# Performance work log

Measured on AMD Instinct MI355X. Metric: run time of the kernel, lower is better.

Reference implementation:

```python
import jax, jax.numpy as jnp
import numpy as np

N = 50000      # nodes
D = 64         # hidden
EMB = 16       # emb_dims
E = 800000     # edges = N * knn(16)
R2 = 0.3 ** 2  # r^2 at epoch 0
GW = 1.0       # grav_weight at epoch 0
EPS = 1e-5


def _lin_params(k, fi, fo):
    kw, kb = jax.random.split(k)
    W = jax.random.normal(kw, (fi, fo), jnp.float32) / np.sqrt(fi).astype(np.float32)
    b = jax.random.normal(kb, (fo,), jnp.float32) * 0.01
    return W, b


def setup_inputs() -> dict:
    key = jax.random.key(0)
    ks = jax.random.split(key, 16)
    inp = {}
    inp['hidden_features'] = jax.random.normal(ks[0], (N, D), jnp.float32)
    inp['edge_index'] = jax.random.randint(ks[1], (2, E), 0, N, jnp.int32)
    inp['current_epoch'] = 0
    # spatial network: (D+1)->D->D->EMB, each Linear + LayerNorm + ReLU
    for i, (fi, fo) in enumerate([(D + 1, D), (D, D), (D, EMB)]):
        W, b = _lin_params(ks[2 + i], fi, fo)
        inp[f'sW{i}'] = W
        inp[f'sb{i}'] = b
        inp[f'sg{i}'] = jnp.ones((fo,), jnp.float32)
        inp[f'sB{i}'] = jnp.zeros((fo,), jnp.float32)
    # feature network: 2*(D+1)->D->D, each Linear + LayerNorm + ReLU
    for i, (fi, fo) in enumerate([(2 * (D + 1), D), (D, D)]):
        W, b = _lin_params(ks[8 + i], fi, fo)
        inp[f'fW{i}'] = W
        inp[f'fb{i}'] = b
        inp[f'fg{i}'] = jnp.ones((fo,), jnp.float32)
        inp[f'fB{i}'] = jnp.zeros((fo,), jnp.float32)
    return inp


def _ln(x, g, b):
    m = jnp.mean(x, axis=-1, keepdims=True)
    v = jnp.mean((x - m) ** 2, axis=-1, keepdims=True)
    return (x - m) * jax.lax.rsqrt(v + EPS) * g + b


def _blk(x, W, b, g, B):
    return jax.nn.relu(_ln(x @ W + b, g, B))


def reference(hidden_features, edge_index, current_epoch,
              sW0, sb0, sg0, sB0, sW1, sb1, sg1, sB1, sW2, sb2, sg2, sB2,
              fW0, fb0, fg0, fB0, fW1, fb1, fg1, fB1):
    # append per-node mean channel: [N, D] -> [N, D+1]
    h = jnp.concatenate([hidden_features,
                         jnp.mean(hidden_features, axis=1, keepdims=True)], axis=-1)
    # spatial embedding [N, EMB]
    s = _blk(_blk(_blk(h, sW0, sb0, sg0, sB0), sW1, sb1, sg1, sB1), sW2, sb2, sg2, sB2)
    start = edge_index[0]
    end = edge_index[1]
    # gravitational edge weight: exp(-grav_weight * ||s_i - s_j||^2 / r^2)
    d = jnp.sum((s[start] - s[end]) ** 2, axis=-1)  # [E]
    w = jnp.exp(-GW * d / R2)                        # [E]
    # gather -> weight -> scatter_add aggregation
    agg = jax.ops.segment_sum(h[start] * w[:, None], end, num_segments=h.shape[0])
    cat = jnp.concatenate([agg, h], axis=-1)  # [N, 2*(D+1)]
    out = _blk(_blk(cat, fW0, fb0, fg0, fB0), fW1, fb1, fg1, fB1)  # [N, D]
    return out, s
```

## Files before the change

kernel.cpp:

```cpp
#include <hip/hip_runtime.h>
#include <hip/hip_bf16.h>
#include <hip/hip_fp16.h>

#define NN 50000
#define DD 64
#define EMBD 16
#define EE 800000
#define CAP 48
#define TILES ((NN + 63) / 64)
#define AGGB ((NN + 3) / 4)

#define OW_S0 0
#define OW_S1 6656
#define OW_S2 11264
#define OW_F0 12416
#define OW_F1 23168
#define NWB   27776

typedef short s16x8 __attribute__((ext_vector_type(8)));
typedef float f32x4 __attribute__((ext_vector_type(4)));
typedef _Float16 h16x8 __attribute__((ext_vector_type(8)));

__device__ __forceinline__ float bcast(float v, int l) {
  return __int_as_float(__builtin_amdgcn_readlane(__float_as_int(v), l));
}

__device__ __forceinline__ unsigned short f2b(float x) {
  unsigned u = __float_as_uint(x);
  return (unsigned short)((u + 0x7FFFu + ((u >> 16) & 1u)) >> 16);
}

__device__ __forceinline__ float b2f(unsigned short u) {
  return __uint_as_float(((unsigned)u) << 16);
}

__device__ __forceinline__ unsigned short f2h(float x) {
  return __half_as_ushort(__float2half(x));
}

__device__ __forceinline__ float h2f(unsigned short u) {
  return (float)__ushort_as_half(u);
}

__device__ __forceinline__ float wred64f(float v) {
  v += __shfl_xor(v, 1);  v += __shfl_xor(v, 2);  v += __shfl_xor(v, 4);
  v += __shfl_xor(v, 8);  v += __shfl_xor(v, 16); v += __shfl_xor(v, 32);
  return v;
}

__global__ __launch_bounds__(256)
void GravConv3556_prep_k(const float* __restrict__ sW0, const float* __restrict__ sW1,
                         const float* __restrict__ sW2, const float* __restrict__ fW0,
                         const float* __restrict__ fW1,
                         unsigned short* __restrict__ wb, int* __restrict__ cnt)
{
  int i0 = blockIdx.x * 256 + threadIdx.x;
  int st = gridDim.x * 256;
  for (int i = i0; i < NN; i += st) cnt[i] = 0;
  for (int i = i0; i < 64 * 104; i += st) {
    int n = i / 104, k = i % 104;
    wb[OW_S0 + i] = (k < 65) ? f2b(sW0[k * 64 + n]) : (unsigned short)0;
  }
  for (int i = i0; i < 64 * 72; i += st) {
    int n = i / 72, k = i % 72;
    wb[OW_S1 + i] = (k < 64) ? f2b(sW1[k * 64 + n]) : (unsigned short)0;
  }
  for (int i = i0; i < 16 * 72; i += st) {
    int n = i / 72, k = i % 72;
    wb[OW_S2 + i] = (k < 64) ? f2b(sW2[k * 16 + n]) : (unsigned short)0;
  }
  for (int i = i0; i < 64 * 168; i += st) {
    int n = i / 168, k = i % 168;
    wb[OW_F0 + i] = (k < 130) ? f2b(fW0[k * 64 + n]) : (unsigned short)0;
  }
  for (int i = i0; i < 64 * 72; i += st) {
    int n = i / 72, k = i % 72;
    wb[OW_F1 + i] = (k < 64) ? f2b(fW1[k * 64 + n]) : (unsigned short)0;
  }
}

#define XROW 104
__global__ __launch_bounds__(256)
void GravConv3556_spatial_k(const float* __restrict__ hidden,
    const unsigned short* __restrict__ wb,
    const float* __restrict__ sb0, const float* __restrict__ sg0, const float* __restrict__ sB0,
    const float* __restrict__ sb1, const float* __restrict__ sg1, const float* __restrict__ sB1,
    const float* __restrict__ sb2, const float* __restrict__ sg2, const float* __restrict__ sB2,
    float* __restrict__ s_out, unsigned short* __restrict__ s16,
    unsigned short* __restrict__ hid16)
{
  __shared__ unsigned short X[64 * XROW];
  __shared__ unsigned short W0[64 * XROW];
  __shared__ unsigned short W1[64 * 72];
  __shared__ unsigned short W2[16 * 72];
  int tid = threadIdx.x;
  int lane = tid & 63;
  int wv = tid >> 6;
  int c = lane & 15;
  int q = lane >> 4;
  int base = blockIdx.x * 64;

  {
    const uint4* g = (const uint4*)(wb + OW_S0); uint4* l = (uint4*)W0;
    for (int i = tid; i < 832; i += 256) l[i] = g[i];
    g = (const uint4*)(wb + OW_S1); l = (uint4*)W1;
    for (int i = tid; i < 576; i += 256) l[i] = g[i];
    g = (const uint4*)(wb + OW_S2); l = (uint4*)W2;
    for (int i = tid; i < 144; i += 256) l[i] = g[i];
  }
  for (int i = 0; i < 16; i++) {
    int m = wv * 16 + i;
    int node = base + m; if (node >= NN) node = NN - 1;
    float x = hidden[(size_t)node * 64 + lane];
    float mean = wred64f(x) * (1.0f / 64.0f);
    X[m * XROW + lane] = f2b(x);
    hid16[(size_t)node * 64 + lane] = f2h(x);
    if (lane == 0) X[m * XROW + 64] = f2b(mean);
    if (lane < 39) X[m * XROW + 65 + lane] = 0;
  }
  __syncthreads();

  int mrow = wv * 16 + c;
  float z[16];

  {
    s16x8 a[3];
    #pragma unroll
    for (int kc = 0; kc < 3; kc++)
      a[kc] = *(const s16x8*)(X + mrow * XROW + kc * 32 + q * 8);
    #pragma unroll
    for (int nt = 0; nt < 4; nt++) {
      f32x4 acc = {0.f, 0.f, 0.f, 0.f};
      #pragma unroll
      for (int kc = 0; kc < 3; kc++) {
        s16x8 b = *(const s16x8*)(W0 + (nt * 16 + c) * XROW + kc * 32 + q * 8);
        acc = __builtin_amdgcn_mfma_f32_16x16x32_bf16(a[kc], b, acc, 0, 0, 0);
      }
      float bias = sb0[nt * 16 + c];
      #pragma unroll
      for (int reg = 0; reg < 4; reg++) z[nt * 4 + reg] = acc[reg] + bias;
    }
    #pragma unroll
    for (int reg = 0; reg < 4; reg++) {
      float s1 = z[reg] + z[4 + reg] + z[8 + reg] + z[12 + reg];
      float s2 = z[reg] * z[reg] + z[4 + reg] * z[4 + reg]
               + z[8 + reg] * z[8 + reg] + z[12 + reg] * z[12 + reg];
      s1 += __shfl_xor(s1, 1); s2 += __shfl_xor(s2, 1);
      s1 += __shfl_xor(s1, 2); s2 += __shfl_xor(s2, 2);
      s1 += __shfl_xor(s1, 4); s2 += __shfl_xor(s2, 4);
      s1 += __shfl_xor(s1, 8); s2 += __shfl_xor(s2, 8);
      float mu = s1 * (1.0f / 64.0f);
      float rs = rsqrtf(fmaxf(s2 * (1.0f / 64.0f) - mu * mu, 0.f) + 1e-5f);
      int m = wv * 16 + q * 4 + reg;
      #pragma unroll
      for (int nt = 0; nt < 4; nt++) {
        int n = nt * 16 + c;
        float y = fmaxf(fmaf((z[nt * 4 + reg] - mu) * rs, sg0[n], sB0[n]), 0.f);
        X[m * XROW + n] = f2b(y);
      }
    }
  }

  {
    s16x8 a[2];
    #pragma unroll
    for (int kc = 0; kc < 2; kc++)
      a[kc] = *(const s16x8*)(X + mrow * XROW + kc * 32 + q * 8);
    #pragma unroll
    for (int nt = 0; nt < 4; nt++) {
      f32x4 acc = {0.f, 0.f, 0.f, 0.f};
      #pragma unroll
      for (int kc = 0; kc < 2; kc++) {
        s16x8 b = *(const s16x8*)(W1 + (nt * 16 + c) * 72 + kc * 32 + q * 8);
        acc = __builtin_amdgcn_mfma_f32_16x16x32_bf16(a[kc], b, acc, 0, 0, 0);
      }
      float bias = sb1[nt * 16 + c];
      #pragma unroll
      for (int reg = 0; reg < 4; reg++) z[nt * 4 + reg] = acc[reg] + bias;
    }
    #pragma unroll
    for (int reg = 0; reg < 4; reg++) {
      float s1 = z[reg] + z[4 + reg] + z[8 + reg] + z[12 + reg];
      float s2 = z[reg] * z[reg] + z[4 + reg] * z[4 + reg]
               + z[8 + reg] * z[8 + reg] + z[12 + reg] * z[12 + reg];
      s1 += __shfl_xor(s1, 1); s2 += __shfl_xor(s2, 1);
      s1 += __shfl_xor(s1, 2); s2 += __shfl_xor(s2, 2);
      s1 += __shfl_xor(s1, 4); s2 += __shfl_xor(s2, 4);
      s1 += __shfl_xor(s1, 8); s2 += __shfl_xor(s2, 8);
      float mu = s1 * (1.0f / 64.0f);
      float rs = rsqrtf(fmaxf(s2 * (1.0f / 64.0f) - mu * mu, 0.f) + 1e-5f);
      int m = wv * 16 + q * 4 + reg;
      #pragma unroll
      for (int nt = 0; nt < 4; nt++) {
        int n = nt * 16 + c;
        float y = fmaxf(fmaf((z[nt * 4 + reg] - mu) * rs, sg1[n], sB1[n]), 0.f);
        X[m * XROW + n] = f2b(y);
      }
    }
  }

  {
    s16x8 a[2];
    #pragma unroll
    for (int kc = 0; kc < 2; kc++)
      a[kc] = *(const s16x8*)(X + mrow * XROW + kc * 32 + q * 8);
    f32x4 acc = {0.f, 0.f, 0.f, 0.f};
    #pragma unroll
    for (int kc = 0; kc < 2; kc++) {
      s16x8 b = *(const s16x8*)(W2 + c * 72 + kc * 32 + q * 8);
      acc = __builtin_amdgcn_mfma_f32_16x16x32_bf16(a[kc], b, acc, 0, 0, 0);
    }
    float bias = sb2[c];
    float z4[4];
    #pragma unroll
    for (int reg = 0; reg < 4; reg++) z4[reg] = acc[reg] + bias;
    #pragma unroll
    for (int reg = 0; reg < 4; reg++) {
      float s1 = z4[reg], s2 = z4[reg] * z4[reg];
      s1 += __shfl_xor(s1, 1); s2 += __shfl_xor(s2, 1);
      s1 += __shfl_xor(s1, 2); s2 += __shfl_xor(s2, 2);
      s1 += __shfl_xor(s1, 4); s2 += __shfl_xor(s2, 4);
      s1 += __shfl_xor(s1, 8); s2 += __shfl_xor(s2, 8);
      float mu = s1 * (1.0f / 16.0f);
      float rs = rsqrtf(fmaxf(s2 * (1.0f / 16.0f) - mu * mu, 0.f) + 1e-5f);
      float y = fmaxf(fmaf((z4[reg] - mu) * rs, sg2[c], sB2[c]), 0.f);
      int node = base + wv * 16 + q * 4 + reg;
      if (node < NN) {
        s_out[(size_t)node * 16 + c] = y;
        s16[(size_t)node * 16 + c] = f2h(y);
      }
    }
  }
}

__global__ __launch_bounds__(256)
void GravConv3556_scatter_k(const int* __restrict__ ei, const unsigned short* __restrict__ s16,
                            int* __restrict__ cnt, unsigned* __restrict__ pairs)
{
  int e = blockIdx.x * 256 + threadIdx.x;
  if (e >= EE) return;
  int a = ei[e];
  int b = ei[EE + e];
  const _Float16* s = (const _Float16*)s16;
  const h16x8* sa = (const h16x8*)(s + (size_t)a * 16);
  const h16x8* sb = (const h16x8*)(s + (size_t)b * 16);
  h16x8 p0 = sa[0], p1 = sa[1];
  h16x8 q0 = sb[0], q1 = sb[1];
  float d = 0.f;
  #pragma unroll
  for (int t = 0; t < 8; t++) {
    float u = (float)p0[t] - (float)q0[t];
    d = fmaf(u, u, d);
    float v = (float)p1[t] - (float)q1[t];
    d = fmaf(v, v, d);
  }
  float w = __expf(d * (-1.0f / 0.09f));
  int pos = atomicAdd(&cnt[b], 1);
  if (pos < CAP)
    pairs[(size_t)b * CAP + pos] = ((unsigned)a << 16) | (unsigned)f2h(w);
}

__global__ __launch_bounds__(256)
void GravConv3556_agg_k(const unsigned short* __restrict__ hid16,
                        const int* __restrict__ cnt, const unsigned* __restrict__ pairs,
                        unsigned short* __restrict__ aggr)
{
  int lane = threadIdx.x & 63;
  int n = blockIdx.x * 4 + (threadIdx.x >> 6);
  if (n >= NN) return;
  const _Float16* hid = (const _Float16*)hid16;
  int m = cnt[n]; if (m > CAP) m = CAP;
  float xa0 = 0.f, xa1 = 0.f, xa2 = 0.f, xa3 = 0.f;
  unsigned pr = 0;
  if (lane < m) pr = pairs[(size_t)n * CAP + lane];
#define GSTEP(q, ACC) { int jj = jb + (q); int jc = jj < m ? jj : m - 1;        \
    unsigned u_ = (unsigned)__builtin_amdgcn_readlane((int)pr, jc);             \
    int   a_ = (int)(u_ >> 16);                                                 \
    float w_ = (jj < m) ? h2f((unsigned short)(u_ & 0xFFFFu)) : 0.0f;           \
    ACC = fmaf(w_, (float)hid[(size_t)a_ * 64 + lane], ACC); }
  for (int jb = 0; jb < m; jb += 8) {
    GSTEP(0, xa0) GSTEP(1, xa1) GSTEP(2, xa2) GSTEP(3, xa3)
    GSTEP(4, xa0) GSTEP(5, xa1) GSTEP(6, xa2) GSTEP(7, xa3)
  }
#undef GSTEP
  aggr[(size_t)n * 64 + lane] = f2b((xa0 + xa1) + (xa2 + xa3));
}

#define CROW 168
__global__ __launch_bounds__(256)
void GravConv3556_feature_k(const float* __restrict__ hidden,
    const unsigned short* __restrict__ aggr, const unsigned short* __restrict__ wb,
    const float* __restrict__ fb0, const float* __restrict__ fg0, const float* __restrict__ fB0,
    const float* __restrict__ fb1, const float* __restrict__ fg1, const float* __restrict__ fB1,
    float* __restrict__ out)
{
  __shared__ unsigned short catB[64 * CROW];
  __shared__ unsigned short W0T[64 * CROW];
  __shared__ unsigned short W1T[64 * 72];
  int tid = threadIdx.x;
  int lane = tid & 63;
  int wv = tid >> 6;
  int c = lane & 15;
  int q = lane >> 4;
  int base = blockIdx.x * 64;

  {
    const uint4* g = (const uint4*)(wb + OW_F0); uint4* l = (uint4*)W0T;
    for (int i = tid; i < 1344; i += 256) l[i] = g[i];
    g = (const uint4*)(wb + OW_F1); l = (uint4*)W1T;
    for (int i = tid; i < 576; i += 256) l[i] = g[i];
  }

  for (int i = 0; i < 16; i++) {
    int m = wv * 16 + i;
    int node = base + m; if (node >= NN) node = NN - 1;
    unsigned short ra = aggr[(size_t)node * 64 + lane];
    float xa = b2f(ra);
    float mA = wred64f(xa) * (1.0f / 64.0f);
    catB[m * CROW + lane] = ra;
    float xh = hidden[(size_t)node * 64 + lane];
    float mB = wred64f(xh) * (1.0f / 64.0f);
    catB[m * CROW + 65 + lane] = f2b(xh);
    if (lane == 0) {
      catB[m * CROW + 64] = f2b(mA);
      catB[m * CROW + 129] = f2b(mB);
    }
    if (lane < 38) catB[m * CROW + 130 + lane] = 0;
  }
  __syncthreads();

  int mrow = wv * 16 + c;

  s16x8 a0[5];
  #pragma unroll
  for (int kc = 0; kc < 5; kc++)
    a0[kc] = *(const s16x8*)(catB + mrow * CROW + kc * 32 + q * 8);

  float z[16];
  #pragma unroll
  for (int nt = 0; nt < 4; nt++) {
    f32x4 acc = {0.f, 0.f, 0.f, 0.f};
    #pragma unroll
    for (int kc = 0; kc < 5; kc++) {
      s16x8 b = *(const s16x8*)(W0T + (nt * 16 + c) * CROW + kc * 32 + q * 8);
      acc = __builtin_amdgcn_mfma_f32_16x16x32_bf16(a0[kc], b, acc, 0, 0, 0);
    }
    float bias = fb0[nt * 16 + c];
    #pragma unroll
    for (int reg = 0; reg < 4; reg++) z[nt * 4 + reg] = acc[reg] + bias;
  }
  #pragma unroll
  for (int reg = 0; reg < 4; reg++) {
    float s1 = z[reg] + z[4 + reg] + z[8 + reg] + z[12 + reg];
    float s2 = z[reg] * z[reg] + z[4 + reg] * z[4 + reg]
             + z[8 + reg] * z[8 + reg] + z[12 + reg] * z[12 + reg];
    s1 += __shfl_xor(s1, 1); s2 += __shfl_xor(s2, 1);
    s1 += __shfl_xor(s1, 2); s2 += __shfl_xor(s2, 2);
    s1 += __shfl_xor(s1, 4); s2 += __shfl_xor(s2, 4);
    s1 += __shfl_xor(s1, 8); s2 += __shfl_xor(s2, 8);
    float mu = s1 * (1.0f / 64.0f);
    float rs = rsqrtf(fmaxf(s2 * (1.0f / 64.0f) - mu * mu, 0.f) + 1e-5f);
    int m = wv * 16 + q * 4 + reg;
    #pragma unroll
    for (int nt = 0; nt < 4; nt++) {
      int n = nt * 16 + c;
      float y = fmaxf(fmaf((z[nt * 4 + reg] - mu) * rs, fg0[n], fB0[n]), 0.f);
      catB[m * CROW + n] = f2b(y);
    }
  }

  s16x8 a1[2];
  #pragma unroll
  for (int kc = 0; kc < 2; kc++)
    a1[kc] = *(const s16x8*)(catB + mrow * CROW + kc * 32 + q * 8);

  #pragma unroll
  for (int nt = 0; nt < 4; nt++) {
    f32x4 acc = {0.f, 0.f, 0.f, 0.f};
    #pragma unroll
    for (int kc = 0; kc < 2; kc++) {
      s16x8 b = *(const s16x8*)(W1T + (nt * 16 + c) * 72 + kc * 32 + q * 8);
      acc = __builtin_amdgcn_mfma_f32_16x16x32_bf16(a1[kc], b, acc, 0, 0, 0);
    }
    float bias = fb1[nt * 16 + c];
    #pragma unroll
    for (int reg = 0; reg < 4; reg++) z[nt * 4 + reg] = acc[reg] + bias;
  }
  #pragma unroll
  for (int reg = 0; reg < 4; reg++) {
    float s1 = z[reg] + z[4 + reg] + z[8 + reg] + z[12 + reg];
    float s2 = z[reg] * z[reg] + z[4 + reg] * z[4 + reg]
             + z[8 + reg] * z[8 + reg] + z[12 + reg] * z[12 + reg];
    s1 += __shfl_xor(s1, 1); s2 += __shfl_xor(s2, 1);
    s1 += __shfl_xor(s1, 2); s2 += __shfl_xor(s2, 2);
    s1 += __shfl_xor(s1, 4); s2 += __shfl_xor(s2, 4);
    s1 += __shfl_xor(s1, 8); s2 += __shfl_xor(s2, 8);
    float mu = s1 * (1.0f / 64.0f);
    float rs = rsqrtf(fmaxf(s2 * (1.0f / 64.0f) - mu * mu, 0.f) + 1e-5f);
    int node = base + wv * 16 + q * 4 + reg;
    if (node < NN) {
      #pragma unroll
      for (int nt = 0; nt < 4; nt++) {
        int n = nt * 16 + c;
        float y = fmaxf(fmaf((z[nt * 4 + reg] - mu) * rs, fg1[n], fB1[n]), 0.f);
        out[(size_t)node * 64 + n] = y;
      }
    }
  }
}

extern "C" void kernel_launch(void* const* d_in, const int* in_sizes, int n_in,
                              void* d_out, int out_size, void* d_ws, size_t ws_size,
                              hipStream_t stream) {
  const float* hidden = (const float*)d_in[0];
  const int*   ei     = (const int*)d_in[1];
  const float *sW0 = (const float*)d_in[3],  *sb0 = (const float*)d_in[4],
              *sg0 = (const float*)d_in[5],  *sB0 = (const float*)d_in[6];
  const float *sW1 = (const float*)d_in[7],  *sb1 = (const float*)d_in[8],
              *sg1 = (const float*)d_in[9],  *sB1 = (const float*)d_in[10];
  const float *sW2 = (const float*)d_in[11], *sb2 = (const float*)d_in[12],
              *sg2 = (const float*)d_in[13], *sB2 = (const float*)d_in[14];
  const float *fW0 = (const float*)d_in[15], *fb0 = (const float*)d_in[16],
              *fg0 = (const float*)d_in[17], *fB0 = (const float*)d_in[18];
  const float *fW1 = (const float*)d_in[19], *fb1 = (const float*)d_in[20],
              *fg1 = (const float*)d_in[21], *fB1 = (const float*)d_in[22];

  float* out   = (float*)d_out;
  float* s_out = out + (size_t)NN * 64;

  unsigned* pairs = (unsigned*)d_ws;
  int*   cnt   = (int*)(pairs + (size_t)NN * CAP);
  unsigned short* aggr  = (unsigned short*)(cnt + NN);
  unsigned short* hid16 = aggr + (size_t)NN * 64;
  unsigned short* s16   = hid16 + (size_t)NN * 64;
  unsigned short* wbuf  = s16 + (size_t)NN * 16;

  GravConv3556_prep_k<<<64, 256, 0, stream>>>(sW0, sW1, sW2, fW0, fW1, wbuf, cnt);
  GravConv3556_spatial_k<<<TILES, 256, 0, stream>>>(hidden, wbuf,
      sb0, sg0, sB0, sb1, sg1, sB1, sb2, sg2, sB2, s_out, s16, hid16);
  GravConv3556_scatter_k<<<(EE + 255) / 256, 256, 0, stream>>>(ei, s16, cnt, pairs);
  GravConv3556_agg_k<<<AGGB, 256, 0, stream>>>(hid16, cnt, pairs, aggr);
  GravConv3556_feature_k<<<TILES, 256, 0, stream>>>(hidden, aggr, wbuf,
      fb0, fg0, fB0, fb1, fg1, fB1, out);
}
```

Before: 227.2 us.

## Split edge bucketing into sliced counters and move weight computation into aggregation

The edge scatter now only buckets source indices per destination, storing 16-bit indices in 8 per-slice buckets so atomics contend less. It runs before the spatial network because it no longer needs embeddings. The Gaussian edge weight is computed inside the aggregation kernel, where each lane gathers its neighbour's embedding. This costs an extra per-lane embedding gather and a prefix over the slice counts in aggregation, and it drops edges when a slice overflows its 16-entry capacity or a node has more than 64 total.

```diff
diff --git a/kernel.cpp b/kernel.cpp
--- a/kernel.cpp
+++ b/kernel.cpp
@@ -6,7 +6,8 @@
 #define DD 64
 #define EMBD 16
 #define EE 800000
-#define CAP 48
+#define SLICES 8
+#define SCAP 16
 #define TILES ((NN + 63) / 64)
 #define AGGB ((NN + 3) / 4)
 
@@ -52,11 +53,11 @@
 void GravConv3556_prep_k(const float* __restrict__ sW0, const float* __restrict__ sW1,
                          const float* __restrict__ sW2, const float* __restrict__ fW0,
                          const float* __restrict__ fW1,
-                         unsigned short* __restrict__ wb, int* __restrict__ cnt)
+                         unsigned short* __restrict__ wb, int* __restrict__ cntx)
 {
   int i0 = blockIdx.x * 256 + threadIdx.x;
   int st = gridDim.x * 256;
-  for (int i = i0; i < NN; i += st) cnt[i] = 0;
+  for (int i = i0; i < SLICES * NN; i += st) cntx[i] = 0;
   for (int i = i0; i < 64 * 104; i += st) {
     int n = i / 104, k = i % 104;
     wb[OW_S0 + i] = (k < 65) ? f2b(sW0[k * 64 + n]) : (unsigned short)0;
@@ -76,6 +77,21 @@
   for (int i = i0; i < 64 * 72; i += st) {
     int n = i / 72, k = i % 72;
     wb[OW_F1 + i] = (k < 64) ? f2b(fW1[k * 64 + n]) : (unsigned short)0;
+  }
+}
+
+__global__ __launch_bounds__(256)
+void GravConv3556_scatter_k(const int* __restrict__ ei, int* __restrict__ cntx,
+                            unsigned short* __restrict__ pairsx)
+{
+  int slice = blockIdx.x & 7;
+  int* cnt = cntx + slice * NN;
+  unsigned short* px = pairsx + (size_t)slice * NN * SCAP;
+  for (int e = blockIdx.x * 256 + threadIdx.x; e < EE; e += gridDim.x * 256) {
+    int a = ei[e];
+    int b = ei[EE + e];
+    int pos = atomicAdd(&cnt[b], 1);
+    if (pos < SCAP) px[b * SCAP + pos] = (unsigned short)a;
   }
 }
 
@@ -234,45 +250,54 @@
 }
 
 __global__ __launch_bounds__(256)
-void GravConv3556_scatter_k(const int* __restrict__ ei, const unsigned short* __restrict__ s16,
-                            int* __restrict__ cnt, unsigned* __restrict__ pairs)
-{
-  int e = blockIdx.x * 256 + threadIdx.x;
-  if (e >= EE) return;
-  int a = ei[e];
-  int b = ei[EE + e];
-  const _Float16* s = (const _Float16*)s16;
-  const h16x8* sa = (const h16x8*)(s + (size_t)a * 16);
-  const h16x8* sb = (const h16x8*)(s + (size_t)b * 16);
-  h16x8 p0 = sa[0], p1 = sa[1];
-  h16x8 q0 = sb[0], q1 = sb[1];
-  float d = 0.f;
-  #pragma unroll
-  for (int t = 0; t < 8; t++) {
-    float u = (float)p0[t] - (float)q0[t];
-    d = fmaf(u, u, d);
-    float v = (float)p1[t] - (float)q1[t];
-    d = fmaf(v, v, d);
-  }
-  float w = __expf(d * (-1.0f / 0.09f));
-  int pos = atomicAdd(&cnt[b], 1);
-  if (pos < CAP)
-    pairs[(size_t)b * CAP + pos] = ((unsigned)a << 16) | (unsigned)f2h(w);
-}
-
-__global__ __launch_bounds__(256)
 void GravConv3556_agg_k(const unsigned short* __restrict__ hid16,
-                        const int* __restrict__ cnt, const unsigned* __restrict__ pairs,
+                        const unsigned short* __restrict__ s16,
+                        const int* __restrict__ cntx,
+                        const unsigned short* __restrict__ pairsx,
                         unsigned short* __restrict__ aggr)
 {
   int lane = threadIdx.x & 63;
   int n = blockIdx.x * 4 + (threadIdx.x >> 6);
   if (n >= NN) return;
   const _Float16* hid = (const _Float16*)hid16;
-  int m = cnt[n]; if (m > CAP) m = CAP;
+  const _Float16* s = (const _Float16*)s16;
+
+  int cs = 0;
+  if (lane < 8) {
+    cs = cntx[lane * NN + n];
+    cs = cs < SCAP ? cs : SCAP;
+  }
+  int s_id = 0, loc = 0, m = 0;
+  {
+    int off = 0;
+    #pragma unroll
+    for (int k = 0; k < 8; k++) {
+      int ck = __shfl(cs, k);
+      if (lane >= off && lane < off + ck) { s_id = k; loc = lane - off; }
+      off += ck;
+    }
+    m = off < 64 ? off : 64;
+  }
+  unsigned pr = 0;
+  if (lane < m) {
+    int a = pairsx[(size_t)s_id * NN * SCAP + (size_t)n * SCAP + loc];
+    const h16x8* sa = (const h16x8*)(s + (size_t)a * 16);
+    const h16x8* sn = (const h16x8*)(s + (size_t)n * 16);
+    h16x8 p0 = sa[0], p1 = sa[1];
+    h16x8 q0 = sn[0], q1 = sn[1];
+    float d = 0.f;
+    #pragma unroll
+    for (int t = 0; t < 8; t++) {
+      float u = (float)p0[t] - (float)q0[t];
+      d = fmaf(u, u, d);
+      float v = (float)p1[t] - (float)q1[t];
+      d = fmaf(v, v, d);
+    }
+    float w = __expf(d * (-1.0f / 0.09f));
+    pr = ((unsigned)a << 16) | (unsigned)f2h(w);
+  }
+
   float xa0 = 0.f, xa1 = 0.f, xa2 = 0.f, xa3 = 0.f;
-  unsigned pr = 0;
-  if (lane < m) pr = pairs[(size_t)n * CAP + lane];
 #define GSTEP(q, ACC) { int jj = jb + (q); int jc = jj < m ? jj : m - 1;        \
     unsigned u_ = (unsigned)__builtin_amdgcn_readlane((int)pr, jc);             \
     int   a_ = (int)(u_ >> 16);                                                 \
@@ -428,18 +453,18 @@
   float* out   = (float*)d_out;
   float* s_out = out + (size_t)NN * 64;
 
-  unsigned* pairs = (unsigned*)d_ws;
-  int*   cnt   = (int*)(pairs + (size_t)NN * CAP);
-  unsigned short* aggr  = (unsigned short*)(cnt + NN);
+  unsigned short* pairsx = (unsigned short*)d_ws;
+  int* cntx = (int*)(pairsx + (size_t)SLICES * NN * SCAP);
+  unsigned short* aggr  = (unsigned short*)(cntx + SLICES * NN);
   unsigned short* hid16 = aggr + (size_t)NN * 64;
   unsigned short* s16   = hid16 + (size_t)NN * 64;
   unsigned short* wbuf  = s16 + (size_t)NN * 16;
 
-  GravConv3556_prep_k<<<64, 256, 0, stream>>>(sW0, sW1, sW2, fW0, fW1, wbuf, cnt);
+  GravConv3556_prep_k<<<128, 256, 0, stream>>>(sW0, sW1, sW2, fW0, fW1, wbuf, cntx);
+  GravConv3556_scatter_k<<<1024, 256, 0, stream>>>(ei, cntx, pairsx);
   GravConv3556_spatial_k<<<TILES, 256, 0, stream>>>(hidden, wbuf,
       sb0, sg0, sB0, sb1, sg1, sB1, sb2, sg2, sB2, s_out, s16, hid16);
-  GravConv3556_scatter_k<<<(EE + 255) / 256, 256, 0, stream>>>(ei, s16, cnt, pairs);
-  GravConv3556_agg_k<<<AGGB, 256, 0, stream>>>(hid16, cnt, pairs, aggr);
+  GravConv3556_agg_k<<<AGGB, 256, 0, stream>>>(hid16, s16, cntx, pairsx, aggr);
   GravConv3556_feature_k<<<TILES, 256, 0, stream>>>(hidden, aggr, wbuf,
       fb0, fg0, fB0, fb1, fg1, fB1, out);
 }
```

Result: no change. 228.6 us (+0.6%).

## Replace global atomic bucketing with per-block LDS bucketing and fuse edge weights into aggregation

Applied to the files above, without the earlier changes.

Drops the separate scatter kernel, which used global atomics to bucket edges by destination. Each of 256 aggregation blocks now scans the whole 16-bit compacted destination list, buckets edges for its own 196 nodes in LDS, computes the gravitational weights in place, and then gathers. This removes the global atomics, the pairs buffer and one launch. In exchange every block rereads the full destination array (about 1.6 MB each, 256 times), and per-node in-degree is capped at 64.

```diff
diff --git a/kernel.cpp b/kernel.cpp
--- a/kernel.cpp
+++ b/kernel.cpp
@@ -6,9 +6,10 @@
 #define DD 64
 #define EMBD 16
 #define EE 800000
-#define CAP 48
 #define TILES ((NN + 63) / 64)
-#define AGGB ((NN + 3) / 4)
+#define NB 256
+#define NPB 196
+#define LCAP 64
 
 #define OW_S0 0
 #define OW_S1 6656
@@ -21,10 +22,6 @@
 typedef float f32x4 __attribute__((ext_vector_type(4)));
 typedef _Float16 h16x8 __attribute__((ext_vector_type(8)));
 
-__device__ __forceinline__ float bcast(float v, int l) {
-  return __int_as_float(__builtin_amdgcn_readlane(__float_as_int(v), l));
-}
-
 __device__ __forceinline__ unsigned short f2b(float x) {
   unsigned u = __float_as_uint(x);
   return (unsigned short)((u + 0x7FFFu + ((u >> 16) & 1u)) >> 16);
@@ -51,12 +48,17 @@
 __global__ __launch_bounds__(256)
 void GravConv3556_prep_k(const float* __restrict__ sW0, const float* __restrict__ sW1,
                          const float* __restrict__ sW2, const float* __restrict__ fW0,
-                         const float* __restrict__ fW1,
-                         unsigned short* __restrict__ wb, int* __restrict__ cnt)
+                         const float* __restrict__ fW1, const int* __restrict__ ei,
+                         unsigned short* __restrict__ wb,
+                         unsigned short* __restrict__ src16,
+                         unsigned short* __restrict__ dst16)
 {
   int i0 = blockIdx.x * 256 + threadIdx.x;
   int st = gridDim.x * 256;
-  for (int i = i0; i < NN; i += st) cnt[i] = 0;
+  for (int i = i0; i < EE; i += st) {
+    src16[i] = (unsigned short)ei[i];
+    dst16[i] = (unsigned short)ei[EE + i];
+  }
   for (int i = i0; i < 64 * 104; i += st) {
     int n = i / 104, k = i % 104;
     wb[OW_S0 + i] = (k < 65) ? f2b(sW0[k * 64 + n]) : (unsigned short)0;
@@ -233,57 +235,78 @@
   }
 }
 
-__global__ __launch_bounds__(256)
-void GravConv3556_scatter_k(const int* __restrict__ ei, const unsigned short* __restrict__ s16,
-                            int* __restrict__ cnt, unsigned* __restrict__ pairs)
-{
-  int e = blockIdx.x * 256 + threadIdx.x;
-  if (e >= EE) return;
-  int a = ei[e];
-  int b = ei[EE + e];
-  const _Float16* s = (const _Float16*)s16;
-  const h16x8* sa = (const h16x8*)(s + (size_t)a * 16);
-  const h16x8* sb = (const h16x8*)(s + (size_t)b * 16);
-  h16x8 p0 = sa[0], p1 = sa[1];
-  h16x8 q0 = sb[0], q1 = sb[1];
-  float d = 0.f;
-  #pragma unroll
-  for (int t = 0; t < 8; t++) {
-    float u = (float)p0[t] - (float)q0[t];
-    d = fmaf(u, u, d);
-    float v = (float)p1[t] - (float)q1[t];
-    d = fmaf(v, v, d);
-  }
-  float w = __expf(d * (-1.0f / 0.09f));
-  int pos = atomicAdd(&cnt[b], 1);
-  if (pos < CAP)
-    pairs[(size_t)b * CAP + pos] = ((unsigned)a << 16) | (unsigned)f2h(w);
-}
-
-__global__ __launch_bounds__(256)
+__global__ __launch_bounds__(1024)
 void GravConv3556_agg_k(const unsigned short* __restrict__ hid16,
-                        const int* __restrict__ cnt, const unsigned* __restrict__ pairs,
+                        const unsigned short* __restrict__ s16,
+                        const unsigned short* __restrict__ src16,
+                        const unsigned short* __restrict__ dst16,
                         unsigned short* __restrict__ aggr)
 {
-  int lane = threadIdx.x & 63;
-  int n = blockIdx.x * 4 + (threadIdx.x >> 6);
-  if (n >= NN) return;
+  __shared__ unsigned short lbuk[NPB * LCAP];
+  __shared__ int lcnt[NPB];
+  int tid = threadIdx.x;
+  int n0 = blockIdx.x * NPB;
+  int nb = NN - n0; if (nb > NPB) nb = NPB;
+  for (int i = tid; i < NPB; i += 1024) lcnt[i] = 0;
+  __syncthreads();
+
+  const uint4* d4 = (const uint4*)dst16;
+  for (int i = tid; i < EE / 8; i += 1024) {
+    uint4 v = d4[i];
+    unsigned dd[4] = {v.x, v.y, v.z, v.w};
+    #pragma unroll
+    for (int cc = 0; cc < 4; cc++) {
+      #pragma unroll
+      for (int hh = 0; hh < 2; hh++) {
+        int b = (int)((dd[cc] >> (16 * hh)) & 0xFFFFu);
+        unsigned rb = (unsigned)(b - n0);
+        if (rb < (unsigned)nb) {
+          int pos = atomicAdd(&lcnt[rb], 1);
+          if (pos < LCAP) lbuk[rb * LCAP + pos] = src16[i * 8 + cc * 2 + hh];
+        }
+      }
+    }
+  }
+  __syncthreads();
+
+  int lane = tid & 63;
+  int wv = tid >> 6;
   const _Float16* hid = (const _Float16*)hid16;
-  int m = cnt[n]; if (m > CAP) m = CAP;
-  float xa0 = 0.f, xa1 = 0.f, xa2 = 0.f, xa3 = 0.f;
-  unsigned pr = 0;
-  if (lane < m) pr = pairs[(size_t)n * CAP + lane];
+  const _Float16* s = (const _Float16*)s16;
+  for (int rn = wv; rn < nb; rn += 16) {
+    int n = n0 + rn;
+    int m = lcnt[rn]; if (m > LCAP) m = LCAP;
+    unsigned pr = 0;
+    if (lane < m) {
+      int a = lbuk[rn * LCAP + lane];
+      const h16x8* sa = (const h16x8*)(s + (size_t)a * 16);
+      const h16x8* sn = (const h16x8*)(s + (size_t)n * 16);
+      h16x8 p0 = sa[0], p1 = sa[1];
+      h16x8 q0 = sn[0], q1 = sn[1];
+      float d = 0.f;
+      #pragma unroll
+      for (int t = 0; t < 8; t++) {
+        float u = (float)p0[t] - (float)q0[t];
+        d = fmaf(u, u, d);
+        float v = (float)p1[t] - (float)q1[t];
+        d = fmaf(v, v, d);
+      }
+      float w = __expf(d * (-1.0f / 0.09f));
+      pr = ((unsigned)a << 16) | (unsigned)f2h(w);
+    }
+    float xa0 = 0.f, xa1 = 0.f, xa2 = 0.f, xa3 = 0.f;
 #define GSTEP(q, ACC) { int jj = jb + (q); int jc = jj < m ? jj : m - 1;        \
     unsigned u_ = (unsigned)__builtin_amdgcn_readlane((int)pr, jc);             \
     int   a_ = (int)(u_ >> 16);                                                 \
     float w_ = (jj < m) ? h2f((unsigned short)(u_ & 0xFFFFu)) : 0.0f;           \
     ACC = fmaf(w_, (float)hid[(size_t)a_ * 64 + lane], ACC); }
-  for (int jb = 0; jb < m; jb += 8) {
-    GSTEP(0, xa0) GSTEP(1, xa1) GSTEP(2, xa2) GSTEP(3, xa3)
-    GSTEP(4, xa0) GSTEP(5, xa1) GSTEP(6, xa2) GSTEP(7, xa3)
-  }
+    for (int jb = 0; jb < m; jb += 8) {
+      GSTEP(0, xa0) GSTEP(1, xa1) GSTEP(2, xa2) GSTEP(3, xa3)
+      GSTEP(4, xa0) GSTEP(5, xa1) GSTEP(6, xa2) GSTEP(7, xa3)
+    }
 #undef GSTEP
-  aggr[(size_t)n * 64 + lane] = f2b((xa0 + xa1) + (xa2 + xa3));
+    aggr[(size_t)n * 64 + lane] = f2b((xa0 + xa1) + (xa2 + xa3));
+  }
 }
 
 #define CROW 168
@@ -428,18 +451,18 @@
   float* out   = (float*)d_out;
   float* s_out = out + (size_t)NN * 64;
 
-  unsigned* pairs = (unsigned*)d_ws;
-  int*   cnt   = (int*)(pairs + (size_t)NN * CAP);
-  unsigned short* aggr  = (unsigned short*)(cnt + NN);
+  unsigned short* src16 = (unsigned short*)d_ws;
+  unsigned short* dst16 = src16 + EE;
+  unsigned short* aggr  = dst16 + EE;
   unsigned short* hid16 = aggr + (size_t)NN * 64;
   unsigned short* s16   = hid16 + (size_t)NN * 64;
   unsigned short* wbuf  = s16 + (size_t)NN * 16;
 
-  GravConv3556_prep_k<<<64, 256, 0, stream>>>(sW0, sW1, sW2, fW0, fW1, wbuf, cnt);
+  GravConv3556_prep_k<<<256, 256, 0, stream>>>(sW0, sW1, sW2, fW0, fW1, ei,
+                                               wbuf, src16, dst16);
   GravConv3556_spatial_k<<<TILES, 256, 0, stream>>>(hidden, wbuf,
       sb0, sg0, sB0, sb1, sg1, sB1, sb2, sg2, sB2, s_out, s16, hid16);
-  GravConv3556_scatter_k<<<(EE + 255) / 256, 256, 0, stream>>>(ei, s16, cnt, pairs);
-  GravConv3556_agg_k<<<AGGB, 256, 0, stream>>>(hid16, cnt, pairs, aggr);
+  GravConv3556_agg_k<<<NB, 1024, 0, stream>>>(hid16, s16, src16, dst16, aggr);
   GravConv3556_feature_k<<<TILES, 256, 0, stream>>>(hidden, aggr, wbuf,
       fb0, fg0, fB0, fb1, fg1, fB1, out);
 }
```

After: 278.6 us. +22.6%, slower.
